# Performance work log

Hardware: AMD Instinct MI355X
Metric: run time of the kernel (lower is better)

## Reference

```python
import jax, jax.numpy as jnp
import numpy as np

B, N, DEG = 16, 2048, 16          # graphs, nodes per graph, avg out-degree
C_IN, HID, K = 64, 128, 32        # in_channels, hidden_channels, out_channels (clusters)
NT = B * N                        # total nodes
E = NT * DEG                      # total edges
GN_EPS = 1e-5


def setup_inputs() -> dict:
    key = jax.random.key(0)
    ks = jax.random.split(key, 6)
    x = jax.random.normal(ks[0], (NT, C_IN), jnp.float32)
    # within-graph random edges (sorted batch => node i belongs to graph i // N)
    src_l = jax.random.randint(ks[1], (E,), 0, N)
    dst_l = jax.random.randint(ks[2], (E,), 0, N)
    gid = jnp.repeat(jnp.arange(B, dtype=jnp.int32), N * DEG)
    edge_index = jnp.stack([gid * N + src_l, gid * N + dst_l]).astype(jnp.int32)
    batch = jnp.repeat(jnp.arange(B, dtype=jnp.int32), N)
    return dict(
        x=x, edge_index=edge_index, batch=batch,
        gn_weight=jnp.ones((C_IN,), jnp.float32),
        gn_bias=jnp.zeros((C_IN,), jnp.float32),
        gn_mean_scale=jnp.ones((C_IN,), jnp.float32),
        w1=jax.random.normal(ks[3], (C_IN, HID), jnp.float32) / np.float32(np.sqrt(C_IN)),
        b1=jnp.zeros((HID,), jnp.float32),
        w2=jax.random.normal(ks[4], (HID, K), jnp.float32) / np.float32(np.sqrt(HID)),
        b2=jnp.zeros((K,), jnp.float32),
    )


def reference(x, gn_weight, gn_bias, gn_mean_scale, w1, b1, w2, b2, edge_index, batch):
    # ---- GraphNorm (per-graph mean/var with learnable mean scale) ----
    ones_n = jnp.ones((NT,), x.dtype)
    cnt = jax.ops.segment_sum(ones_n, batch, num_segments=B)[:, None]        # [B,1]
    mean = jax.ops.segment_sum(x, batch, num_segments=B) / cnt              # [B,C]
    xm = x - gn_mean_scale * mean[batch]
    var = jax.ops.segment_sum(xm * xm, batch, num_segments=B) / cnt         # [B,C]
    h = gn_weight * xm / jnp.sqrt(var + GN_EPS)[batch] + gn_bias            # [NT,C_IN]

    # ---- GCNConv (add self-loops, symmetric D^-1/2 (A+I) D^-1/2) ----
    src, dst = edge_index[0], edge_index[1]
    loop = jnp.arange(NT, dtype=src.dtype)
    src_l = jnp.concatenate([src, loop])
    dst_l = jnp.concatenate([dst, loop])
    deg = jax.ops.segment_sum(jnp.ones_like(src_l, x.dtype), dst_l, num_segments=NT)
    dinv = jnp.where(deg > 0, jax.lax.rsqrt(deg), 0.0)
    norm = dinv[src_l] * dinv[dst_l]                                        # [E+NT]
    hw = h @ w1                                                             # [NT,HID]
    h = jax.ops.segment_sum(norm[:, None] * hw[src_l], dst_l, num_segments=NT) + b1
    h = jax.nn.selu(h)

    # ---- to_dense_batch / to_dense_adj (uniform graph sizes -> mask all True) ----
    xd = h.reshape(B, N, HID)                                               # [B,N,F]
    adj = jnp.zeros((B, N, N), x.dtype).at[batch[src], src % N, dst % N].add(1.0)

    # ---- DMoNPooling ----
    s = jax.nn.softmax(xd @ w2 + b2, axis=-1)                               # [B,N,K]
    out = jax.nn.selu(jnp.einsum('bnk,bnf->bkf', s, xd))                    # [B,K,F]
    sta = jnp.einsum('bnk,bnm->bkm', s, adj)                                # [B,K,N]
    out_adj = jnp.einsum('bkm,bml->bkl', sta, s)                            # [B,K,K]

    degrees = adj.sum(-1)                                                   # [B,N]
    m = degrees.sum(-1) / 2                                                 # [B]
    ca = jnp.einsum('bnk,bn->bk', s, degrees)                               # [B,K]
    normalizer = ca[:, :, None] * ca[:, None, :] / 2 / m[:, None, None]
    spectral_loss = (-jnp.einsum('bkk->b', out_adj - normalizer) / (2 * m)).mean()

    ss = jnp.einsum('bnk,bnl->bkl', s, s)                                   # [B,K,K]
    ss_fro = jnp.sqrt(jnp.sum(ss * ss, axis=(-2, -1), keepdims=True))
    eye = jnp.eye(K, dtype=x.dtype)
    diff = ss / ss_fro - eye / jnp.sqrt(jnp.float32(K))
    ortho_loss = jnp.sqrt(jnp.sum(diff * diff, axis=(-2, -1))).mean()

    cluster_size = s.sum(1)                                                 # [B,K]
    cluster_loss = (jnp.linalg.norm(cluster_size, axis=1) / N
                    * jnp.sqrt(jnp.float32(K)) - 1).mean()
    # (coarsened-adj renormalization in DMoNPooling is unused by Net's outputs)

    return jax.nn.log_softmax(out, axis=-1), spectral_loss + ortho_loss + cluster_loss, s
```

## Files before the change

kernel.cpp:

```cpp
#include <hip/hip_runtime.h>
#include <cmath>

static constexpr int B_  = 16;
static constexpr int N_  = 2048;
static constexpr int NT_ = 32768;
static constexpr int E_  = 524288;

static constexpr size_t OFF_HSC    = 0;
static constexpr size_t OFF_XD     = 2097152;
static constexpr size_t OFF_SWS    = 6291456;
static constexpr size_t OFF_PART   = 7340032;
static constexpr size_t OFF_GSP    = 9437184;
static constexpr size_t OFF_GSP2   = 9445376;
static constexpr size_t OFF_SSP    = 9453568;
static constexpr size_t OFF_CAP    = 9977856;
static constexpr size_t OFF_CSP    = 9994240;
static constexpr size_t OFF_DINV   = 10011136;
static constexpr size_t OFF_IHIN   = 10043904;
static constexpr size_t OFF_IHOUT  = 10306048;
static constexpr size_t OFF_ICURS  = 10568192;
static constexpr size_t OFF_IROWS  = 10830336;
static constexpr size_t OFF_ICNTO  = 10863108;
static constexpr size_t OFF_IESRC  = 10895876;

__device__ __forceinline__ float selu_f(float x) {
  return 1.0507009873554805f * (x > 0.f ? x : 1.6732632423543772f * expm1f(x));
}

__device__ __forceinline__ float block_sum_bcast(float v, float* sm) {
  int lane = threadIdx.x & 63, w = threadIdx.x >> 6;
#pragma unroll
  for (int off = 32; off; off >>= 1) v += __shfl_down(v, off);
  __syncthreads();
  if (lane == 0) sm[w] = v;
  __syncthreads();
  return sm[0] + sm[1] + sm[2] + sm[3];
}

__global__ __launch_bounds__(1024) void k_count(const int* ei, const float* x,
                                                int* histin, int* histout,
                                                float* gsp, float* gsp2) {
  __shared__ int hin[2048], hout[2048];
  __shared__ float l1[16][64], l2[16][64];
  int blk = blockIdx.x;
  int tid = threadIdx.x;
  if (blk < 128) {
    int g = blk >> 3, p = blk & 7;
    int nbase = g * 2048, ebase = g * 32768 + p * 4096;
    hin[tid] = 0; hin[tid + 1024] = 0;
    hout[tid] = 0; hout[tid + 1024] = 0;
    __syncthreads();
#pragma unroll
    for (int it = 0; it < 4; it++) {
      int e = ebase + it * 1024 + tid;
      int s = ei[e], d = ei[E_ + e];
      atomicAdd(&hout[s - nbase], 1);
      atomicAdd(&hin[d - nbase], 1);
    }
    __syncthreads();
    histin[blk * 2048 + tid] = hin[tid];
    histin[blk * 2048 + tid + 1024] = hin[tid + 1024];
    histout[blk * 2048 + tid] = hout[tid];
    histout[blk * 2048 + tid + 1024] = hout[tid + 1024];
  } else {
    int gi = blk - 128;
    int b = gi >> 3, chunk = gi & 7;
    int c = tid & 63, r = tid >> 6;
    float s = 0.f, s2 = 0.f;
    const float* xb = x + ((size_t)b * N_ + (size_t)chunk * 256) * 64;
    for (int n = r; n < 256; n += 16) {
      float v = xb[n * 64 + c];
      s += v; s2 += v * v;
    }
    l1[r][c] = s; l2[r][c] = s2;
    __syncthreads();
    if (r == 0) {
      float t1 = 0.f, t2 = 0.f;
#pragma unroll
      for (int i = 0; i < 16; i++) { t1 += l1[i][c]; t2 += l2[i][c]; }
      gsp[gi * 64 + c] = t1;
      gsp2[gi * 64 + c] = t2;
    }
  }
}

__global__ __launch_bounds__(1024) void k_scan(const int* histin, const int* histout,
                                               int* rows, int* cursp, int* cout_,
                                               float* dinv) {
  __shared__ int wsum[16], woff[16];
  int g = blockIdx.x, tid = threadIdx.x;
  int nbase = g * 2048, ebase = g * 32768;
  int n0 = 2 * tid, n1 = 2 * tid + 1;
  int h0[8], h1[8];
  int a = 0, b = 0, o0 = 0, o1 = 0;
#pragma unroll
  for (int p = 0; p < 8; p++) {
    h0[p] = histin[(g * 8 + p) * 2048 + n0];
    h1[p] = histin[(g * 8 + p) * 2048 + n1];
    a += h0[p]; b += h1[p];
    o0 += histout[(g * 8 + p) * 2048 + n0];
    o1 += histout[(g * 8 + p) * 2048 + n1];
  }
  int tot = a + b;
  int lane = tid & 63, w = tid >> 6;
  int incl = tot;
#pragma unroll
  for (int off = 1; off < 64; off <<= 1) {
    int t = __shfl_up(incl, off);
    if (lane >= off) incl += t;
  }
  if (lane == 63) wsum[w] = incl;
  __syncthreads();
  if (tid < 16) {
    int v = wsum[tid], iv = v;
#pragma unroll
    for (int off = 1; off < 16; off <<= 1) {
      int t = __shfl_up(iv, off, 16);
      if (tid >= off) iv += t;
    }
    woff[tid] = iv - v;
  }
  __syncthreads();
  int pref = incl - tot + woff[w];
  int r0 = ebase + pref, r1 = r0 + a;
  rows[nbase + n0] = r0;
  rows[nbase + n1] = r1;
  dinv[nbase + n0] = rsqrtf((float)(a + 1));
  dinv[nbase + n1] = rsqrtf((float)(b + 1));
  cout_[nbase + n0] = o0;
  cout_[nbase + n1] = o1;
  int run0 = r0, run1 = r1;
#pragma unroll
  for (int p = 0; p < 8; p++) {
    cursp[(g * 8 + p) * 2048 + n0] = run0; run0 += h0[p];
    cursp[(g * 8 + p) * 2048 + n1] = run1; run1 += h1[p];
  }
  if (g == 15 && tid == 1023) rows[NT_] = E_;
}

__global__ __launch_bounds__(256) void k_prepb(const float* x, const float* gsp,
                                               const float* gsp2, const float* gw,
                                               const float* gb, const float* gms,
                                               const float* dinv, float* hsc,
                                               const int* ei, const int* cursp,
                                               int* esrc) {
  __shared__ float shs[64], scs[64];
  __shared__ int cur[2048];
  int tid = threadIdx.x;
  int blk = blockIdx.x;
  if (blk < 2048) {
    int bgr = blk >> 7;
    if (tid < 64) {
      float s = 0.f, s2 = 0.f;
#pragma unroll
      for (int c8 = 0; c8 < 8; c8++) {
        s  += gsp[(bgr * 8 + c8) * 64 + tid];
        s2 += gsp2[(bgr * 8 + c8) * 64 + tid];
      }
      float mean = s * (1.f / 2048.f);
      float a = gms[tid];
      float var = s2 * (1.f / 2048.f) - (2.f * a - a * a) * mean * mean;
      shs[tid] = a * mean;
      scs[tid] = gw[tid] * rsqrtf(var + 1e-5f);
    }
    __syncthreads();
    int idx = blk * 256 + tid;
    int node = idx >> 4, g4 = (idx & 15) * 4;
    float di = dinv[node];
    float4 xv = *(const float4*)&x[(size_t)node * 64 + g4];
    float4 bb = *(const float4*)&gb[g4];
    float4 o;
    o.x = ((xv.x - shs[g4])     * scs[g4]     + bb.x) * di;
    o.y = ((xv.y - shs[g4 + 1]) * scs[g4 + 1] + bb.y) * di;
    o.z = ((xv.z - shs[g4 + 2]) * scs[g4 + 2] + bb.z) * di;
    o.w = ((xv.w - shs[g4 + 3]) * scs[g4 + 3] + bb.w) * di;
    *(float4*)&hsc[(size_t)node * 64 + g4] = o;
  } else {
    int bb = blk - 2048;
    int g = bb >> 3, p = bb & 7;
    int nbase = g * 2048;
    int ebase = g * 32768 + p * 4096;
    for (int i = tid; i < 2048; i += 256) cur[i] = cursp[bb * 2048 + i];
    __syncthreads();
#pragma unroll
    for (int it = 0; it < 16; it++) {
      int e = ebase + it * 256 + tid;
      int s = ei[e], d = ei[E_ + e];
      int pos = atomicAdd(&cur[d - nbase], 1);
      esrc[pos] = s;
    }
  }
}

__global__ __launch_bounds__(256) void k_mm1(const float* hsc, const float* dinv,
                                             const int* rows, const int* esrc,
                                             const float* w1, const float* b1,
                                             float* xd) {
  __shared__ float at[32 * 65];
  int tid = threadIdx.x;
  int n0 = blockIdx.x * 32;
  int wv = tid >> 6, c = tid & 63;
#pragma unroll 1
  for (int i = 0; i < 8; i++) {
    int nn = i * 4 + wv;
    int node = n0 + nn;
    int e0 = rows[node], e1 = rows[node + 1];
    float dd = dinv[node];
    float acc = hsc[(size_t)node * 64 + c];
    for (int e = e0; e < e1; e += 8) {
      int sidx[8]; float wt[8], hv[8];
#pragma unroll
      for (int j = 0; j < 8; j++) {
        int ee = e + j;
        sidx[j] = esrc[ee < e1 ? ee : e0];
        wt[j] = (ee < e1) ? 1.f : 0.f;
      }
#pragma unroll
      for (int j = 0; j < 8; j++) hv[j] = hsc[(size_t)sidx[j] * 64 + c];
#pragma unroll
      for (int j = 0; j < 8; j++) acc += wt[j] * hv[j];
    }
    at[nn * 65 + c] = dd * acc;
  }
  __syncthreads();
  int tx = tid & 31, ty = tid >> 5;
  int f0 = tx * 4, nn = ty * 4;
  float acc[4][4] = {};
  for (int k = 0; k < 64; k++) {
    float4 wvv = *(const float4*)&w1[k * 128 + f0];
#pragma unroll
    for (int i = 0; i < 4; i++) {
      float av = at[(nn + i) * 65 + k];
      acc[i][0] += av * wvv.x; acc[i][1] += av * wvv.y;
      acc[i][2] += av * wvv.z; acc[i][3] += av * wvv.w;
    }
  }
  float4 bv = *(const float4*)&b1[f0];
#pragma unroll
  for (int i = 0; i < 4; i++) {
    float4 o;
    o.x = selu_f(acc[i][0] + bv.x);
    o.y = selu_f(acc[i][1] + bv.y);
    o.z = selu_f(acc[i][2] + bv.z);
    o.w = selu_f(acc[i][3] + bv.w);
    *(float4*)&xd[(size_t)(n0 + nn + i) * 128 + f0] = o;
  }
}

__global__ __launch_bounds__(256) void k_mm2f(const float* xd, const float* w2,
                                              const float* b2, const int* cout_,
                                              float* outs, float* ssp,
                                              float* cap, float* csp, float* part) {
  __shared__ float xt[64 * 129];
  __shared__ float st[64 * 33];
  __shared__ float r1[8][32], r2[8][32];
  int tid = threadIdx.x;
  int blk = blockIdx.x;
  int n0 = blk * 64;
  for (int i = tid; i < 2048; i += 256) {
    int n = i >> 5, j4 = (i & 31) * 4;
    float4 v = *(const float4*)&xd[(size_t)(n0 + n) * 128 + j4];
    xt[n * 129 + j4] = v.x; xt[n * 129 + j4 + 1] = v.y;
    xt[n * 129 + j4 + 2] = v.z; xt[n * 129 + j4 + 3] = v.w;
  }
  __syncthreads();
  int ty = tid >> 3;
  int k0 = (tid & 7) * 4;
  float acc2[2][4] = {};
  for (int j = 0; j < 128; j++) {
    float4 wv = *(const float4*)&w2[j * 32 + k0];
    float x0 = xt[(ty * 2) * 129 + j];
    float x1 = xt[(ty * 2 + 1) * 129 + j];
    acc2[0][0] += x0 * wv.x; acc2[0][1] += x0 * wv.y; acc2[0][2] += x0 * wv.z; acc2[0][3] += x0 * wv.w;
    acc2[1][0] += x1 * wv.x; acc2[1][1] += x1 * wv.y; acc2[1][2] += x1 * wv.z; acc2[1][3] += x1 * wv.w;
  }
  float4 bv2 = *(const float4*)&b2[k0];
#pragma unroll
  for (int i = 0; i < 2; i++) {
    int n = ty * 2 + i;
    st[n * 33 + k0]     = acc2[i][0] + bv2.x;
    st[n * 33 + k0 + 1] = acc2[i][1] + bv2.y;
    st[n * 33 + k0 + 2] = acc2[i][2] + bv2.z;
    st[n * 33 + k0 + 3] = acc2[i][3] + bv2.w;
  }
  __syncthreads();
  {
    int n = tid >> 2, q = (tid & 3) * 8;
    float m = -3.4e38f;
#pragma unroll
    for (int j = 0; j < 8; j++) m = fmaxf(m, st[n * 33 + q + j]);
#pragma unroll
    for (int off = 1; off < 4; off <<= 1) m = fmaxf(m, __shfl_xor(m, off, 4));
    float ev[8]; float ssum = 0.f;
#pragma unroll
    for (int j = 0; j < 8; j++) { ev[j] = expf(st[n * 33 + q + j] - m); ssum += ev[j]; }
#pragma unroll
    for (int off = 1; off < 4; off <<= 1) ssum += __shfl_xor(ssum, off, 4);
    float inv = 1.f / ssum;
#pragma unroll
    for (int j = 0; j < 8; j++) st[n * 33 + q + j] = ev[j] * inv;
  }
  __syncthreads();
  for (int i = tid; i < 512; i += 256) {
    int n = i >> 3, q = (i & 7) * 4;
    float* op = &outs[(size_t)(n0 + n) * 32 + q];
    op[0] = st[n * 33 + q];
    op[1] = st[n * 33 + q + 1];
    op[2] = st[n * 33 + q + 2];
    op[3] = st[n * 33 + q + 3];
  }
  {
    int k = tid >> 3, l0 = (tid & 7) * 4;
    float a0 = 0, a1 = 0, a2 = 0, a3 = 0;
    for (int n = 0; n < 64; n++) {
      float sk = st[n * 33 + k];
      a0 += sk * st[n * 33 + l0];     a1 += sk * st[n * 33 + l0 + 1];
      a2 += sk * st[n * 33 + l0 + 2]; a3 += sk * st[n * 33 + l0 + 3];
    }
    float4 o = {a0, a1, a2, a3};
    *(float4*)&ssp[(size_t)blk * 1024 + k * 32 + l0] = o;
  }
  {
    int k2 = tid & 31, r = tid >> 5;
    float aca = 0.f, acs = 0.f;
    for (int i = 0; i < 8; i++) {
      int n = i * 8 + r;
      float dg = (float)cout_[n0 + n];
      float v = st[n * 33 + k2];
      acs += v; aca += v * dg;
    }
    r1[r][k2] = aca; r2[r][k2] = acs;
    __syncthreads();
    if (r == 0) {
      float sa = 0.f, sc = 0.f;
#pragma unroll
      for (int i = 0; i < 8; i++) { sa += r1[i][k2]; sc += r2[i][k2]; }
      cap[blk * 32 + k2] = sa;
      csp[blk * 32 + k2] = sc;
    }
  }
  {
    int tx = tid & 31, ty2 = tid >> 5;
    int f0 = tx * 4, kk0 = ty2 * 4;
    float acc[4][4] = {};
    for (int n = 0; n < 64; n++) {
      float s0 = st[n * 33 + kk0], s1 = st[n * 33 + kk0 + 1];
      float s2 = st[n * 33 + kk0 + 2], s3 = st[n * 33 + kk0 + 3];
      float4 xv = {xt[n * 129 + f0], xt[n * 129 + f0 + 1], xt[n * 129 + f0 + 2], xt[n * 129 + f0 + 3]};
      acc[0][0] += s0 * xv.x; acc[0][1] += s0 * xv.y; acc[0][2] += s0 * xv.z; acc[0][3] += s0 * xv.w;
      acc[1][0] += s1 * xv.x; acc[1][1] += s1 * xv.y; acc[1][2] += s1 * xv.z; acc[1][3] += s1 * xv.w;
      acc[2][0] += s2 * xv.x; acc[2][1] += s2 * xv.y; acc[2][2] += s2 * xv.z; acc[2][3] += s2 * xv.w;
      acc[3][0] += s3 * xv.x; acc[3][1] += s3 * xv.y; acc[3][2] += s3 * xv.z; acc[3][3] += s3 * xv.w;
    }
#pragma unroll
    for (int i = 0; i < 4; i++) {
      float4 o = {acc[i][0], acc[i][1], acc[i][2], acc[i][3]};
      *(float4*)&part[(size_t)(blk * 32 + kk0 + i) * 128 + f0] = o;
    }
  }
}

__global__ __launch_bounds__(256) void k_spec(const int* rows, const int* esrc,
                                              const float* s, float* specp,
                                              float* lossp) {
  __shared__ float sm8[8];
  int blk = blockIdx.x, tid = threadIdx.x;
  if (blk == 0 && tid == 0) lossp[0] = 0.f;
  int grp = tid >> 5, k = tid & 31;
  int n0 = blk * 32 + grp * 4;
  float acc = 0.f;
#pragma unroll 1
  for (int i = 0; i < 4; i++) {
    int node = n0 + i;
    int e0 = rows[node], e1 = rows[node + 1];
    float sd = s[(size_t)node * 32 + k];
    float agg = 0.f;
    for (int e = e0; e < e1; e += 4) {
      int si[4]; float wt[4], sv[4];
#pragma unroll
      for (int j = 0; j < 4; j++) {
        int ee = e + j;
        si[j] = esrc[ee < e1 ? ee : e0];
        wt[j] = (ee < e1) ? 1.f : 0.f;
      }
#pragma unroll
      for (int j = 0; j < 4; j++) sv[j] = s[(size_t)si[j] * 32 + k];
#pragma unroll
      for (int j = 0; j < 4; j++) agg += wt[j] * sv[j];
    }
    acc += sd * agg;
  }
#pragma unroll
  for (int off = 16; off; off >>= 1) acc += __shfl_down(acc, off, 32);
  if (k == 0) sm8[grp] = acc;
  __syncthreads();
  if (tid == 0) {
    specp[blk] = sm8[0] + sm8[1] + sm8[2] + sm8[3]
               + sm8[4] + sm8[5] + sm8[6] + sm8[7];
  }
}

__global__ __launch_bounds__(256) void k_fin2(const float* part, const float* ssp,
                                              const float* csp, const float* cap,
                                              const float* specp, float* out0,
                                              float* loss) {
  __shared__ float sred[4];
  int blk = blockIdx.x;
  int tid = threadIdx.x;
  if (blk < 256) {
    int half = tid >> 7;
    int f = tid & 127;
    int row = blk * 2 + half;
    int b = row >> 5, k = row & 31;
    float v = 0.f;
#pragma unroll
    for (int c = 0; c < 32; c++) v += part[(size_t)((b * 32 + c) * 32 + k) * 128 + f];
    v = selu_f(v);
    int lane = tid & 63, w = tid >> 6;
    float m = v;
#pragma unroll
    for (int off = 32; off; off >>= 1) m = fmaxf(m, __shfl_down(m, off));
    if (lane == 0) sred[w] = m;
    __syncthreads();
    m = fmaxf(sred[half * 2], sred[half * 2 + 1]);
    float e = expf(v - m);
    float t = e;
    __syncthreads();
#pragma unroll
    for (int off = 32; off; off >>= 1) t += __shfl_down(t, off);
    if (lane == 0) sred[w] = t;
    __syncthreads();
    float tot = sred[half * 2] + sred[half * 2 + 1];
    out0[(size_t)row * 128 + f] = v - m - logf(tot);
  } else {
    int b = blk - 256;
    float v0 = 0, v1 = 0, v2 = 0, v3 = 0;
    for (int c = 0; c < 32; c++) {
      float4 u = *(const float4*)&ssp[(size_t)(b * 32 + c) * 1024 + tid * 4];
      v0 += u.x; v1 += u.y; v2 += u.z; v3 += u.w;
    }
    float ssq = v0 * v0 + v1 * v1 + v2 * v2 + v3 * v3;
    ssq = block_sum_bcast(ssq, sred);
    float inv = 1.f / sqrtf(ssq);
    float dsq = 0.f;
    {
      int i0 = tid * 4;
      float vv[4] = {v0, v1, v2, v3};
#pragma unroll
      for (int jj = 0; jj < 4; jj++) {
        int i = i0 + jj;
        float d = vv[jj] * inv;
        if ((i >> 5) == (i & 31)) d -= 0.17677669529663687f;
        dsq += d * d;
      }
    }
    dsq = block_sum_bcast(dsq, sred);
    float csq = 0.f, casq = 0.f;
    if (tid < 32) {
      float c1 = 0.f, c2 = 0.f;
      for (int c = 0; c < 32; c++) {
        c1 += csp[(size_t)(b * 32 + c) * 32 + tid];
        c2 += cap[(size_t)(b * 32 + c) * 32 + tid];
      }
      csq = c1 * c1; casq = c2 * c2;
    }
    csq = block_sum_bcast(csq, sred);
    casq = block_sum_bcast(casq, sred);
    float spec_sum = (tid < 64) ? specp[b * 64 + tid] : 0.f;
    spec_sum = block_sum_bcast(spec_sum, sred);
    if (tid == 0) {
      float ortho = sqrtf(dsq);
      float cl = sqrtf(csq) * (1.f / 2048.f) * 5.656854249492381f - 1.f;
      float m = 16384.f;
      float spec = -(spec_sum - casq / (2.f * m)) / (2.f * m);
      atomicAdd(loss, (spec + ortho + cl) * (1.f / 16.f));
    }
  }
}

extern "C" void kernel_launch(void* const* d_in, const int* in_sizes, int n_in,
                              void* d_out, int out_size, void* d_ws, size_t ws_size,
                              hipStream_t stream) {
  (void)in_sizes; (void)n_in; (void)out_size; (void)ws_size;
  const float* x   = (const float*)d_in[0];
  const int*   ei  = (const int*)d_in[1];
  const float* gw  = (const float*)d_in[3];
  const float* gb  = (const float*)d_in[4];
  const float* gms = (const float*)d_in[5];
  const float* w1  = (const float*)d_in[6];
  const float* b1  = (const float*)d_in[7];
  const float* w2  = (const float*)d_in[8];
  const float* b2  = (const float*)d_in[9];
  float* out = (float*)d_out;
  float* ws  = (float*)d_ws;

  float* hsc    = ws + OFF_HSC;
  float* xd     = ws + OFF_XD;
  float* part   = ws + OFF_PART;
  float* gsp    = ws + OFF_GSP;
  float* gsp2   = ws + OFF_GSP2;
  float* ssp    = ws + OFF_SSP;
  float* cap    = ws + OFF_CAP;
  float* csp    = ws + OFF_CSP;
  float* specp  = ws + OFF_SWS;
  float* dinv   = ws + OFF_DINV;
  int*   histin = (int*)(ws + OFF_IHIN);
  int*   histout= (int*)(ws + OFF_IHOUT);
  int*   cursp  = (int*)(ws + OFF_ICURS);
  int*   rows   = (int*)(ws + OFF_IROWS);
  int*   cout_  = (int*)(ws + OFF_ICNTO);
  int*   esrc   = (int*)(ws + OFF_IESRC);

  float* out0  = out;
  float* lossp = out + 65536;
  float* outs  = out + 65537;

  hipLaunchKernelGGL(k_count, dim3(256), dim3(1024), 0, stream, ei, x, histin, histout, gsp, gsp2);
  hipLaunchKernelGGL(k_scan, dim3(16), dim3(1024), 0, stream,
                     histin, histout, rows, cursp, cout_, dinv);
  hipLaunchKernelGGL(k_prepb, dim3(2176), dim3(256), 0, stream,
                     x, gsp, gsp2, gw, gb, gms, dinv, hsc, ei, cursp, esrc);
  hipLaunchKernelGGL(k_mm1, dim3(1024), dim3(256), 0, stream, hsc, dinv, rows, esrc, w1, b1, xd);
  hipLaunchKernelGGL(k_mm2f, dim3(512), dim3(256), 0, stream,
                     xd, w2, b2, cout_, outs, ssp, cap, csp, part);
  hipLaunchKernelGGL(k_spec, dim3(1024), dim3(256), 0, stream, rows, esrc, outs, specp, lossp);
  hipLaunchKernelGGL(k_fin2, dim3(272), dim3(256), 0, stream,
                     part, ssp, csp, cap, specp, out0, lossp);
}
```

Baseline: 199.7 us.

## Fold scan into CSR build, fuse spectral and final kernels, XCD-aware block mapping

Removes the separate scan kernel by having each CSR-build block redo the per-graph prefix sum from the histograms in shared memory. dinv is now recomputed from row offsets or histograms instead of stored. The spectral aggregation and finalization kernels are merged into one launch, joined by per-graph atomic counters and a spin-wait. Node blocks in mm1 and spec are remapped so each graph's blocks land on one XCD for L2 locality. This cuts two launches and some intermediate traffic, at the cost of redundant scan work and a spin-wait that can deadlock if the waiting blocks are scheduled before the producer blocks.

```diff
diff --git a/kernel.cpp b/kernel.cpp
--- a/kernel.cpp
+++ b/kernel.cpp
@@ -15,12 +15,9 @@
 static constexpr size_t OFF_SSP    = 9453568;
 static constexpr size_t OFF_CAP    = 9977856;
 static constexpr size_t OFF_CSP    = 9994240;
-static constexpr size_t OFF_DINV   = 10011136;
 static constexpr size_t OFF_IHIN   = 10043904;
 static constexpr size_t OFF_IHOUT  = 10306048;
-static constexpr size_t OFF_ICURS  = 10568192;
 static constexpr size_t OFF_IROWS  = 10830336;
-static constexpr size_t OFF_ICNTO  = 10863108;
 static constexpr size_t OFF_IESRC  = 10895876;
 
 __device__ __forceinline__ float selu_f(float x) {
@@ -84,72 +81,76 @@
   }
 }
 
-__global__ __launch_bounds__(1024) void k_scan(const int* histin, const int* histout,
-                                               int* rows, int* cursp, int* cout_,
-                                               float* dinv) {
-  __shared__ int wsum[16], woff[16];
-  int g = blockIdx.x, tid = threadIdx.x;
-  int nbase = g * 2048, ebase = g * 32768;
-  int n0 = 2 * tid, n1 = 2 * tid + 1;
-  int h0[8], h1[8];
-  int a = 0, b = 0, o0 = 0, o1 = 0;
-#pragma unroll
-  for (int p = 0; p < 8; p++) {
-    h0[p] = histin[(g * 8 + p) * 2048 + n0];
-    h1[p] = histin[(g * 8 + p) * 2048 + n1];
-    a += h0[p]; b += h1[p];
-    o0 += histout[(g * 8 + p) * 2048 + n0];
-    o1 += histout[(g * 8 + p) * 2048 + n1];
-  }
-  int tot = a + b;
-  int lane = tid & 63, w = tid >> 6;
-  int incl = tot;
-#pragma unroll
-  for (int off = 1; off < 64; off <<= 1) {
-    int t = __shfl_up(incl, off);
-    if (lane >= off) incl += t;
-  }
-  if (lane == 63) wsum[w] = incl;
-  __syncthreads();
-  if (tid < 16) {
-    int v = wsum[tid], iv = v;
-#pragma unroll
-    for (int off = 1; off < 16; off <<= 1) {
-      int t = __shfl_up(iv, off, 16);
-      if (tid >= off) iv += t;
-    }
-    woff[tid] = iv - v;
-  }
-  __syncthreads();
-  int pref = incl - tot + woff[w];
-  int r0 = ebase + pref, r1 = r0 + a;
-  rows[nbase + n0] = r0;
-  rows[nbase + n1] = r1;
-  dinv[nbase + n0] = rsqrtf((float)(a + 1));
-  dinv[nbase + n1] = rsqrtf((float)(b + 1));
-  cout_[nbase + n0] = o0;
-  cout_[nbase + n1] = o1;
-  int run0 = r0, run1 = r1;
-#pragma unroll
-  for (int p = 0; p < 8; p++) {
-    cursp[(g * 8 + p) * 2048 + n0] = run0; run0 += h0[p];
-    cursp[(g * 8 + p) * 2048 + n1] = run1; run1 += h1[p];
-  }
-  if (g == 15 && tid == 1023) rows[NT_] = E_;
-}
-
 __global__ __launch_bounds__(256) void k_prepb(const float* x, const float* gsp,
                                                const float* gsp2, const float* gw,
                                                const float* gb, const float* gms,
-                                               const float* dinv, float* hsc,
-                                               const int* ei, const int* cursp,
+                                               float* hsc, const int* ei,
+                                               const int* histin, int* rows,
                                                int* esrc) {
-  __shared__ float shs[64], scs[64];
-  __shared__ int cur[2048];
   int tid = threadIdx.x;
   int blk = blockIdx.x;
-  if (blk < 2048) {
-    int bgr = blk >> 7;
+  if (blk < 128) {
+    __shared__ int tot[2048], cur[2048];
+    __shared__ int wsum[4];
+    int g = blk >> 3, p = blk & 7;
+    int nbase = g * 2048, ebase = g * 32768;
+    for (int i = tid; i < 2048; i += 256) { tot[i] = 0; cur[i] = 0; }
+    __syncthreads();
+    for (int q = 0; q < 8; q++) {
+      const int* hq = &histin[(g * 8 + q) * 2048];
+      for (int i = tid; i < 2048; i += 256) {
+        int v = hq[i];
+        tot[i] += v;
+        if (q < p) cur[i] += v;
+      }
+    }
+    __syncthreads();
+    int base = tid * 8;
+    int loc[8]; int run = 0;
+#pragma unroll
+    for (int j = 0; j < 8; j++) { loc[j] = run; run += tot[base + j]; }
+    int lane = tid & 63, w = tid >> 6;
+    int incl = run;
+#pragma unroll
+    for (int off = 1; off < 64; off <<= 1) {
+      int t = __shfl_up(incl, off);
+      if (lane >= off) incl += t;
+    }
+    if (lane == 63) wsum[w] = incl;
+    __syncthreads();
+    int woffv = 0;
+    for (int k = 0; k < w; k++) woffv += wsum[k];
+    int texcl = incl - run + woffv;
+#pragma unroll
+    for (int j = 0; j < 8; j++) {
+      int pre = cur[base + j];
+      int rv = ebase + texcl + loc[j];
+      if (p == 0) rows[nbase + base + j] = rv;
+      cur[base + j] = rv + pre;
+    }
+    if (p == 0 && g == 15 && tid == 255) rows[NT_] = E_;
+    __syncthreads();
+    int ebp = ebase + p * 4096;
+#pragma unroll
+    for (int it = 0; it < 16; it++) {
+      int e = ebp + it * 256 + tid;
+      int s = ei[e], d = ei[E_ + e];
+      int pos = atomicAdd(&cur[d - nbase], 1);
+      esrc[pos] = s;
+    }
+  } else {
+    __shared__ float shs[64], scs[64], sdin[16];
+    int bb = blk - 128;
+    int bgr = bb >> 7;
+    int nl = (bb & 127) * 16;
+    if (tid < 128) {
+      int node16 = tid >> 3, q = tid & 7;
+      int v = histin[(bgr * 8 + q) * 2048 + nl + node16];
+      v += __shfl_down(v, 4, 8);
+      v += __shfl_down(v, 2, 8);
+      v += __shfl_down(v, 1, 8);
+      if (q == 0) sdin[node16] = rsqrtf((float)(v + 1));
+    }
     if (tid < 64) {
       float s = 0.f, s2 = 0.f;
 #pragma unroll
@@ -164,48 +165,36 @@
       scs[tid] = gw[tid] * rsqrtf(var + 1e-5f);
     }
     __syncthreads();
-    int idx = blk * 256 + tid;
+    int idx = bb * 256 + tid;
     int node = idx >> 4, g4 = (idx & 15) * 4;
-    float di = dinv[node];
+    float di = sdin[tid >> 4];
     float4 xv = *(const float4*)&x[(size_t)node * 64 + g4];
-    float4 bb = *(const float4*)&gb[g4];
+    float4 bbv = *(const float4*)&gb[g4];
     float4 o;
-    o.x = ((xv.x - shs[g4])     * scs[g4]     + bb.x) * di;
-    o.y = ((xv.y - shs[g4 + 1]) * scs[g4 + 1] + bb.y) * di;
-    o.z = ((xv.z - shs[g4 + 2]) * scs[g4 + 2] + bb.z) * di;
-    o.w = ((xv.w - shs[g4 + 3]) * scs[g4 + 3] + bb.w) * di;
+    o.x = ((xv.x - shs[g4])     * scs[g4]     + bbv.x) * di;
+    o.y = ((xv.y - shs[g4 + 1]) * scs[g4 + 1] + bbv.y) * di;
+    o.z = ((xv.z - shs[g4 + 2]) * scs[g4 + 2] + bbv.z) * di;
+    o.w = ((xv.w - shs[g4 + 3]) * scs[g4 + 3] + bbv.w) * di;
     *(float4*)&hsc[(size_t)node * 64 + g4] = o;
-  } else {
-    int bb = blk - 2048;
-    int g = bb >> 3, p = bb & 7;
-    int nbase = g * 2048;
-    int ebase = g * 32768 + p * 4096;
-    for (int i = tid; i < 2048; i += 256) cur[i] = cursp[bb * 2048 + i];
-    __syncthreads();
-#pragma unroll
-    for (int it = 0; it < 16; it++) {
-      int e = ebase + it * 256 + tid;
-      int s = ei[e], d = ei[E_ + e];
-      int pos = atomicAdd(&cur[d - nbase], 1);
-      esrc[pos] = s;
-    }
-  }
-}
-
-__global__ __launch_bounds__(256) void k_mm1(const float* hsc, const float* dinv,
-                                             const int* rows, const int* esrc,
-                                             const float* w1, const float* b1,
-                                             float* xd) {
+  }
+}
+
+__global__ __launch_bounds__(256) void k_mm1(const float* hsc, const int* rows,
+                                             const int* esrc, const float* w1,
+                                             const float* b1, float* xd) {
   __shared__ float at[32 * 65];
   int tid = threadIdx.x;
-  int n0 = blockIdx.x * 32;
+  int bid = blockIdx.x;
+  int xcd = bid & 7, slot = bid >> 3;
+  int g = xcd + ((slot >> 6) << 3);
+  int n0 = g * 2048 + (slot & 63) * 32;
   int wv = tid >> 6, c = tid & 63;
 #pragma unroll 1
   for (int i = 0; i < 8; i++) {
     int nn = i * 4 + wv;
     int node = n0 + nn;
     int e0 = rows[node], e1 = rows[node + 1];
-    float dd = dinv[node];
+    float dd = rsqrtf((float)(e1 - e0 + 1));
     float acc = hsc[(size_t)node * 64 + c];
     for (int e = e0; e < e1; e += 8) {
       int sidx[8]; float wt[8], hv[8];
@@ -248,15 +237,28 @@
 }
 
 __global__ __launch_bounds__(256) void k_mm2f(const float* xd, const float* w2,
-                                              const float* b2, const int* cout_,
+                                              const float* b2, const int* histout,
                                               float* outs, float* ssp,
-                                              float* cap, float* csp, float* part) {
+                                              float* cap, float* csp, float* part,
+                                              float* specg, int* cntg, float* lossp) {
   __shared__ float xt[64 * 129];
   __shared__ float st[64 * 33];
   __shared__ float r1[8][32], r2[8][32];
+  __shared__ float cdeg[64];
   int tid = threadIdx.x;
   int blk = blockIdx.x;
+  if (blk == 0) {
+    if (tid < 16) { specg[tid] = 0.f; cntg[tid] = 0; }
+    else if (tid == 16) lossp[0] = 0.f;
+  }
   int n0 = blk * 64;
+  int g = n0 >> 11, nl0 = n0 & 2047;
+  if (tid < 64) {
+    int ssum = 0;
+#pragma unroll
+    for (int q = 0; q < 8; q++) ssum += histout[(g * 8 + q) * 2048 + nl0 + tid];
+    cdeg[tid] = (float)ssum;
+  }
   for (int i = tid; i < 2048; i += 256) {
     int n = i >> 5, j4 = (i & 31) * 4;
     float4 v = *(const float4*)&xd[(size_t)(n0 + n) * 128 + j4];
@@ -325,7 +327,7 @@
     float aca = 0.f, acs = 0.f;
     for (int i = 0; i < 8; i++) {
       int n = i * 8 + r;
-      float dg = (float)cout_[n0 + n];
+      float dg = cdeg[n];
       float v = st[n * 33 + k2];
       acs += v; aca += v * dg;
     }
@@ -360,57 +362,57 @@
   }
 }
 
-__global__ __launch_bounds__(256) void k_spec(const int* rows, const int* esrc,
-                                              const float* s, float* specp,
-                                              float* lossp) {
-  __shared__ float sm8[8];
+__global__ __launch_bounds__(256) void k_specfin(const int* rows, const int* esrc,
+                                                 const float* s, const float* part,
+                                                 const float* ssp, const float* csp,
+                                                 const float* cap, float* specg,
+                                                 int* cntg, float* out0,
+                                                 float* loss) {
+  __shared__ float smem[8];
   int blk = blockIdx.x, tid = threadIdx.x;
-  if (blk == 0 && tid == 0) lossp[0] = 0.f;
-  int grp = tid >> 5, k = tid & 31;
-  int n0 = blk * 32 + grp * 4;
-  float acc = 0.f;
+  if (blk < 1024) {
+    int xcd = blk & 7, slot = blk >> 3;
+    int g = xcd + ((slot >> 6) << 3);
+    int grp = tid >> 5, k = tid & 31;
+    int n0 = g * 2048 + (slot & 63) * 32 + grp * 4;
+    float acc = 0.f;
 #pragma unroll 1
-  for (int i = 0; i < 4; i++) {
-    int node = n0 + i;
-    int e0 = rows[node], e1 = rows[node + 1];
-    float sd = s[(size_t)node * 32 + k];
-    float agg = 0.f;
-    for (int e = e0; e < e1; e += 4) {
-      int si[4]; float wt[4], sv[4];
-#pragma unroll
-      for (int j = 0; j < 4; j++) {
-        int ee = e + j;
-        si[j] = esrc[ee < e1 ? ee : e0];
-        wt[j] = (ee < e1) ? 1.f : 0.f;
+    for (int i = 0; i < 4; i++) {
+      int node = n0 + i;
+      int e0 = rows[node], e1 = rows[node + 1];
+      float sd = s[(size_t)node * 32 + k];
+      float agg = 0.f;
+      for (int e = e0; e < e1; e += 4) {
+        int si[4]; float wt[4], sv[4];
+#pragma unroll
+        for (int j = 0; j < 4; j++) {
+          int ee = e + j;
+          si[j] = esrc[ee < e1 ? ee : e0];
+          wt[j] = (ee < e1) ? 1.f : 0.f;
+        }
+#pragma unroll
+        for (int j = 0; j < 4; j++) sv[j] = s[(size_t)si[j] * 32 + k];
+#pragma unroll
+        for (int j = 0; j < 4; j++) agg += wt[j] * sv[j];
       }
-#pragma unroll
-      for (int j = 0; j < 4; j++) sv[j] = s[(size_t)si[j] * 32 + k];
-#pragma unroll
-      for (int j = 0; j < 4; j++) agg += wt[j] * sv[j];
-    }
-    acc += sd * agg;
-  }
-#pragma unroll
-  for (int off = 16; off; off >>= 1) acc += __shfl_down(acc, off, 32);
-  if (k == 0) sm8[grp] = acc;
-  __syncthreads();
-  if (tid == 0) {
-    specp[blk] = sm8[0] + sm8[1] + sm8[2] + sm8[3]
-               + sm8[4] + sm8[5] + sm8[6] + sm8[7];
-  }
-}
-
-__global__ __launch_bounds__(256) void k_fin2(const float* part, const float* ssp,
-                                              const float* csp, const float* cap,
-                                              const float* specp, float* out0,
-                                              float* loss) {
-  __shared__ float sred[4];
-  int blk = blockIdx.x;
-  int tid = threadIdx.x;
-  if (blk < 256) {
+      acc += sd * agg;
+    }
+#pragma unroll
+    for (int off = 16; off; off >>= 1) acc += __shfl_down(acc, off, 32);
+    if (k == 0) smem[grp] = acc;
+    __syncthreads();
+    if (tid == 0) {
+      float v = smem[0] + smem[1] + smem[2] + smem[3]
+              + smem[4] + smem[5] + smem[6] + smem[7];
+      atomicAdd(&specg[g], v);
+      __threadfence();
+      atomicAdd(&cntg[g], 1);
+    }
+  } else if (blk < 1280) {
+    int rb = blk - 1024;
     int half = tid >> 7;
     int f = tid & 127;
-    int row = blk * 2 + half;
+    int row = rb * 2 + half;
     int b = row >> 5, k = row & 31;
     float v = 0.f;
 #pragma unroll
@@ -420,27 +422,27 @@
     float m = v;
 #pragma unroll
     for (int off = 32; off; off >>= 1) m = fmaxf(m, __shfl_down(m, off));
-    if (lane == 0) sred[w] = m;
-    __syncthreads();
-    m = fmaxf(sred[half * 2], sred[half * 2 + 1]);
+    if (lane == 0) smem[w] = m;
+    __syncthreads();
+    m = fmaxf(smem[half * 2], smem[half * 2 + 1]);
     float e = expf(v - m);
     float t = e;
     __syncthreads();
 #pragma unroll
     for (int off = 32; off; off >>= 1) t += __shfl_down(t, off);
-    if (lane == 0) sred[w] = t;
-    __syncthreads();
-    float tot = sred[half * 2] + sred[half * 2 + 1];
+    if (lane == 0) smem[w] = t;
+    __syncthreads();
+    float tot = smem[half * 2] + smem[half * 2 + 1];
     out0[(size_t)row * 128 + f] = v - m - logf(tot);
   } else {
-    int b = blk - 256;
+    int b = blk - 1280;
     float v0 = 0, v1 = 0, v2 = 0, v3 = 0;
     for (int c = 0; c < 32; c++) {
       float4 u = *(const float4*)&ssp[(size_t)(b * 32 + c) * 1024 + tid * 4];
       v0 += u.x; v1 += u.y; v2 += u.z; v3 += u.w;
     }
     float ssq = v0 * v0 + v1 * v1 + v2 * v2 + v3 * v3;
-    ssq = block_sum_bcast(ssq, sred);
+    ssq = block_sum_bcast(ssq, smem);
     float inv = 1.f / sqrtf(ssq);
     float dsq = 0.f;
     {
@@ -454,7 +456,7 @@
         dsq += d * d;
       }
     }
-    dsq = block_sum_bcast(dsq, sred);
+    dsq = block_sum_bcast(dsq, smem);
     float csq = 0.f, casq = 0.f;
     if (tid < 32) {
       float c1 = 0.f, c2 = 0.f;
@@ -464,11 +466,11 @@
       }
       csq = c1 * c1; casq = c2 * c2;
     }
-    csq = block_sum_bcast(csq, sred);
-    casq = block_sum_bcast(casq, sred);
-    float spec_sum = (tid < 64) ? specp[b * 64 + tid] : 0.f;
-    spec_sum = block_sum_bcast(spec_sum, sred);
+    csq = block_sum_bcast(csq, smem);
+    casq = block_sum_bcast(casq, smem);
     if (tid == 0) {
+      while (atomicAdd(&cntg[b], 0) < 64) { }
+      float spec_sum = atomicAdd(&specg[b], 0.f);
       float ortho = sqrtf(dsq);
       float cl = sqrtf(csq) * (1.f / 2048.f) * 5.656854249492381f - 1.f;
       float m = 16384.f;
@@ -502,13 +504,11 @@
   float* ssp    = ws + OFF_SSP;
   float* cap    = ws + OFF_CAP;
   float* csp    = ws + OFF_CSP;
-  float* specp  = ws + OFF_SWS;
-  float* dinv   = ws + OFF_DINV;
+  float* specg  = ws + OFF_SWS;
+  int*   cntg   = (int*)(ws + OFF_SWS) + 16;
   int*   histin = (int*)(ws + OFF_IHIN);
   int*   histout= (int*)(ws + OFF_IHOUT);
-  int*   cursp  = (int*)(ws + OFF_ICURS);
   int*   rows   = (int*)(ws + OFF_IROWS);
-  int*   cout_  = (int*)(ws + OFF_ICNTO);
   int*   esrc   = (int*)(ws + OFF_IESRC);
 
   float* out0  = out;
@@ -516,14 +516,11 @@
   float* outs  = out + 65537;
 
   hipLaunchKernelGGL(k_count, dim3(256), dim3(1024), 0, stream, ei, x, histin, histout, gsp, gsp2);
-  hipLaunchKernelGGL(k_scan, dim3(16), dim3(1024), 0, stream,
-                     histin, histout, rows, cursp, cout_, dinv);
   hipLaunchKernelGGL(k_prepb, dim3(2176), dim3(256), 0, stream,
-                     x, gsp, gsp2, gw, gb, gms, dinv, hsc, ei, cursp, esrc);
-  hipLaunchKernelGGL(k_mm1, dim3(1024), dim3(256), 0, stream, hsc, dinv, rows, esrc, w1, b1, xd);
+                     x, gsp, gsp2, gw, gb, gms, hsc, ei, histin, rows, esrc);
+  hipLaunchKernelGGL(k_mm1, dim3(1024), dim3(256), 0, stream, hsc, rows, esrc, w1, b1, xd);
   hipLaunchKernelGGL(k_mm2f, dim3(512), dim3(256), 0, stream,
-                     xd, w2, b2, cout_, outs, ssp, cap, csp, part);
-  hipLaunchKernelGGL(k_spec, dim3(1024), dim3(256), 0, stream, rows, esrc, outs, specp, lossp);
-  hipLaunchKernelGGL(k_fin2, dim3(272), dim3(256), 0, stream,
-                     part, ssp, csp, cap, specp, out0, lossp);
-}
+                     xd, w2, b2, histout, outs, ssp, cap, csp, part, specg, cntg, lossp);
+  hipLaunchKernelGGL(k_specfin, dim3(1296), dim3(256), 0, stream,
+                     rows, esrc, outs, part, ssp, csp, cap, specg, cntg, out0, lossp);
+}
```

Result: slower. 225.6 us (+13.0%).
